# Kernel optimization log

Hardware: AMD Instinct MI355X
Metric: run time of the kernel (lower is better)

## Reference

```python
import jax, jax.numpy as jnp
import numpy as np

B, C, D = 8192, 4, 256
E, H, O = 8, 256, 128
AQ, HQ = 18, 512
THRESH = 0.3
MAX_OUT_REC = 2


def setup_inputs() -> dict:
    key = jax.random.key(0)
    ks = jax.random.split(key, 16)
    s = lambda *sh: 1.0 / np.sqrt(sh[-2] if len(sh) > 1 else sh[-1])
    inp = {
        'data': jax.random.normal(ks[0], (B, C, D), jnp.float32),
        # stacked expert MLPs: D -> H -> O
        'We1': jax.random.normal(ks[1], (E, D, H), jnp.float32) / np.sqrt(D),
        'be1': jnp.zeros((E, H), jnp.float32),
        'We2': jax.random.normal(ks[2], (E, H, O), jnp.float32) / np.sqrt(H),
        'be2': jnp.zeros((E, O), jnp.float32),
        # gating: D -> E (softmax)
        'Wg': jax.random.normal(ks[3], (D, E), jnp.float32) / np.sqrt(D),
        'bg': jnp.zeros((E,), jnp.float32),
        # outer recursive gating: C*O -> 2 (softmax)
        'Wog': jax.random.normal(ks[4], (C * O, 2), jnp.float32) / np.sqrt(C * O),
        'bog': jnp.zeros((2,), jnp.float32),
        # recursive mapping: O -> D
        'Wr': jax.random.normal(ks[5], (O, D), jnp.float32) / np.sqrt(O),
        'br': jnp.zeros((D,), jnp.float32),
        # Q network: C*O -> HQ -> A
        'Wq1': jax.random.normal(ks[6], (C * O, HQ), jnp.float32) / np.sqrt(C * O),
        'bq1': jnp.zeros((HQ,), jnp.float32),
        'Wq2': jax.random.normal(ks[7], (HQ, AQ), jnp.float32) / np.sqrt(HQ),
        'bq2': jnp.zeros((AQ,), jnp.float32),
    }
    return inp


def _moe_forward(x3, We1, be1, We2, be2, Wg, bg):
    # x3: (B, C, D) -> tokens (N, D), N = B*C
    b = x3.shape[0]
    x = x3.reshape(b * C, D)
    # dense all-experts forward
    h = jax.nn.relu(jnp.einsum('nd,edh->enh', x, We1) + be1[:, None, :])  # (E,N,H)
    eo = jnp.einsum('enh,eho->eno', h, We2) + be2[:, None, :]              # (E,N,O)
    g = jax.nn.softmax(x @ Wg + bg, axis=-1)                               # (N,E)
    out = jnp.einsum('ne,eno->no', g, eo)                                  # (N,O)
    return out.reshape(b, C * O)


def reference(data, We1, be1, We2, be2, Wg, bg, Wog, bog, Wr, br, Wq1, bq1, Wq2, bq2):
    result = _moe_forward(data, We1, be1, We2, be2, Wg, bg)               # (B, C*O)
    co = jax.nn.softmax(result @ Wog + bog, axis=-1)                      # (B, 2)
    gate2 = (co[:, 0] > THRESH).astype(result.dtype)[:, None]             # (B, 1)
    # while-loop with per-sample mask; unrolled MAX_OUT_REC iterations is
    # exact: once a sample's mask is 0 its result (hence mask) is unchanged.
    for _ in range(MAX_OUT_REC):
        r_ = result.reshape(data.shape[0] * C, O) @ Wr + br               # recursive_mapping
        r3 = r_.reshape(data.shape[0], C, D)
        out = _moe_forward(r3, We1, be1, We2, be2, Wg, bg)
        result = result + out * co[:, 0:1] * gate2
        co = jax.nn.softmax(result @ Wog + bog, axis=-1)
        gate2 = (co[:, 0] > 0.5).astype(result.dtype)[:, None]
    values = jax.nn.relu(result @ Wq1 + bq1) @ Wq2 + bq2                  # (B, A)
    return values
```

## Files before the change

kernel.cpp:

```cpp
#include <hip/hip_runtime.h>
#include <math.h>


typedef _Float16 f16;
typedef f16   f16x8  __attribute__((ext_vector_type(8)));
typedef f16   f16x4  __attribute__((ext_vector_type(4)));
typedef float f32x16 __attribute__((ext_vector_type(16)));
typedef float v4f    __attribute__((ext_vector_type(4)));

#define MFMA(a, b, c) __builtin_amdgcn_mfma_f32_32x32x16_f16(a, b, c, 0, 0, 0)
#define LO_SCALE 4096.0f
#define LO_INV   (1.0f / 4096.0f)

#define XS 264
#define RS 136
#define QS 520

__device__ __forceinline__ v4f nt_load4(const float* p) {
    return __builtin_nontemporal_load((const v4f*)p);
}

__global__ __launch_bounds__(256) void prep_kernel(
    const float* __restrict__ We1, const float* __restrict__ We2,
    const float* __restrict__ Wr,  const float* __restrict__ Wg,
    const float* __restrict__ Wq1, const float* __restrict__ Wq2,
    f16* __restrict__ W1H, f16* __restrict__ W1L,
    f16* __restrict__ W2H, f16* __restrict__ W2L,
    f16* __restrict__ WrH, f16* __restrict__ WrL,
    f16* __restrict__ WgH, f16* __restrict__ WgL,
    f16* __restrict__ Wq1H, f16* __restrict__ Wq1L,
    f16* __restrict__ Wq2H, f16* __restrict__ Wq2L)
{
    int t = blockIdx.x * 4 + (threadIdx.x >> 6);
    int lane = threadIdx.x & 63;
    const float* src; f16 *dh, *dl;
    int stride, ncols, kbase, nbase, tile;
    if (t < 1024) {
        int e = t >> 7, kt = (t >> 3) & 15, nt = t & 7;
        src = We1 + e * 65536; stride = 256; ncols = 256;
        kbase = kt * 16; nbase = nt * 32; tile = t; dh = W1H; dl = W1L;
    } else if (t < 1536) {
        int i = t - 1024; int e = i >> 6, kt = (i >> 2) & 15, nt = i & 3;
        src = We2 + e * 32768; stride = 128; ncols = 128;
        kbase = kt * 16; nbase = nt * 32; tile = i; dh = W2H; dl = W2L;
    } else if (t < 1600) {
        int i = t - 1536; int kt = i >> 3, nt = i & 7;
        src = Wr; stride = 256; ncols = 256;
        kbase = kt * 16; nbase = nt * 32; tile = i; dh = WrH; dl = WrL;
    } else if (t < 1616) {
        int i = t - 1600;
        src = Wg; stride = 8; ncols = 8;
        kbase = i * 16; nbase = 0; tile = i; dh = WgH; dl = WgL;
    } else if (t < 2128) {
        int i = t - 1616; int kt = i >> 4, nt = i & 15;
        src = Wq1; stride = 512; ncols = 512;
        kbase = kt * 16; nbase = nt * 32; tile = i; dh = Wq1H; dl = Wq1L;
    } else {
        int i = t - 2128;
        src = Wq2; stride = 18; ncols = 18;
        kbase = i * 16; nbase = 0; tile = i; dh = Wq2H; dl = Wq2L;
    }
    int n = lane & 31, kg = lane >> 5;
    int col = nbase + n;
    f16x8 hv, lv;
    #pragma unroll
    for (int j = 0; j < 8; ++j) {
        int k = kbase + kg * 8 + j;
        float w = (col < ncols) ? src[(size_t)k * stride + col] : 0.f;
        f16 h = (f16)w;
        hv[j] = h;
        lv[j] = (f16)((w - (float)h) * LO_SCALE);
    }
    *(f16x8*)(dh + (size_t)tile * 512 + lane * 8) = hv;
    *(f16x8*)(dl + (size_t)tile * 512 + lane * 8) = lv;
}

template<bool REC>
__global__ __launch_bounds__(256, 2) void moe_mfma(
    const float* xsrc, const float* __restrict__ sbuf,
    const f16* __restrict__ W1H, const f16* __restrict__ W1L,
    const f16* __restrict__ W2H, const f16* __restrict__ W2L,
    const f16* __restrict__ WrH, const f16* __restrict__ WrL,
    const f16* __restrict__ WgH, const f16* __restrict__ WgL,
    const float* __restrict__ be1, const float* __restrict__ be2,
    const float* __restrict__ bg,  const float* __restrict__ br,
    float* result)
{
    extern __shared__ char smem[];
    f16* xh = (f16*)smem;
    f16* xl = xh + 32 * XS;
    f16* hh = xl + 32 * XS;
    f16* hl = hh + 32 * XS;

    const int tid = threadIdx.x;
    const int lane = tid & 63;
    const int wv = tid >> 6;
    const int l31 = lane & 31;
    const int kg = lane >> 5;
    const int n0 = blockIdx.x * 32;

    if (!REC) {
        #pragma unroll
        for (int i = 0; i < 8; ++i) {
            int idx = i * 256 + tid;
            int m = idx >> 6, k4 = (idx & 63) * 4;
            v4f v = nt_load4(&xsrc[(size_t)(n0 + m) * 256 + k4]);
            f16x4 hv, lv;
            #pragma unroll
            for (int j = 0; j < 4; ++j) {
                hv[j] = (f16)v[j];
                lv[j] = (f16)((v[j] - (float)hv[j]) * LO_SCALE);
            }
            *(f16x4*)&xh[m * XS + k4] = hv;
            *(f16x4*)&xl[m * XS + k4] = lv;
        }
    } else {
        #pragma unroll
        for (int i = 0; i < 4; ++i) {
            int idx = i * 256 + tid;
            int m = idx >> 5, k4 = (idx & 31) * 4;
            v4f v = nt_load4(&xsrc[(size_t)(n0 + m) * 128 + k4]);
            f16x4 hv, lv;
            #pragma unroll
            for (int j = 0; j < 4; ++j) {
                hv[j] = (f16)v[j];
                lv[j] = (f16)((v[j] - (float)hv[j]) * LO_SCALE);
            }
            *(f16x4*)&hh[m * RS + k4] = hv;
            *(f16x4*)&hl[m * RS + k4] = lv;
        }
        __syncthreads();
        f32x16 am0 = {}, a0a = {}, a0b = {}, am1 = {}, a1a = {}, a1b = {};
        const f16* wrh = WrH + (size_t)(2 * wv) * 512 + lane * 8;
        const f16* wrl = WrL + (size_t)(2 * wv) * 512 + lane * 8;
        #pragma unroll
        for (int kt = 0; kt < 8; ++kt) {
            f16x8 b0h = *(const f16x8*)(wrh + (size_t)kt * 4096);
            f16x8 b0l = *(const f16x8*)(wrl + (size_t)kt * 4096);
            f16x8 b1h = *(const f16x8*)(wrh + (size_t)kt * 4096 + 512);
            f16x8 b1l = *(const f16x8*)(wrl + (size_t)kt * 4096 + 512);
            f16x8 ah = *(const f16x8*)&hh[l31 * RS + kt * 16 + kg * 8];
            f16x8 al = *(const f16x8*)&hl[l31 * RS + kt * 16 + kg * 8];
            am0 = MFMA(ah, b0h, am0); a0a = MFMA(al, b0h, a0a); a0b = MFMA(ah, b0l, a0b);
            am1 = MFMA(ah, b1h, am1); a1a = MFMA(al, b1h, a1a); a1b = MFMA(ah, b1l, a1b);
        }
        #pragma unroll
        for (int t = 0; t < 2; ++t) {
            int col = (2 * wv + t) * 32 + l31;
            float brv = br[col];
            #pragma unroll
            for (int r = 0; r < 16; ++r) {
                int row = (r & 3) + 8 * (r >> 2) + 4 * kg;
                float v = (t ? am1[r] + (a1a[r] + a1b[r]) * LO_INV
                             : am0[r] + (a0a[r] + a0b[r]) * LO_INV) + brv;
                f16 hv = (f16)v;
                xh[row * XS + col] = hv;
                xl[row * XS + col] = (f16)((v - (float)hv) * LO_SCALE);
            }
        }
    }
    __syncthreads();

    float gr[16];
    {
        f32x16 gm = {}, ga = {}, gb = {};
        #pragma unroll
        for (int kt = 0; kt < 16; ++kt) {
            f16x8 ah = *(const f16x8*)&xh[l31 * XS + kt * 16 + kg * 8];
            f16x8 al = *(const f16x8*)&xl[l31 * XS + kt * 16 + kg * 8];
            f16x8 bh = *(const f16x8*)(WgH + (size_t)kt * 512 + lane * 8);
            f16x8 bl = *(const f16x8*)(WgL + (size_t)kt * 512 + lane * 8);
            gm = MFMA(ah, bh, gm); ga = MFMA(al, bh, ga); gb = MFMA(ah, bl, gb);
        }
        float bge = (l31 < 8) ? bg[l31] : 0.f;
        #pragma unroll
        for (int r = 0; r < 16; ++r) {
            float lg = gm[r] + (ga[r] + gb[r]) * LO_INV + bge;
            float mx = lg;
            #pragma unroll
            for (int d = 1; d < 8; d <<= 1) mx = fmaxf(mx, __shfl_xor(mx, d, 64));
            float ex = __expf(lg - mx);
            float s = ex;
            #pragma unroll
            for (int d = 1; d < 8; d <<= 1) s += __shfl_xor(s, d, 64);
            gr[r] = ex / s;
        }
    }

    f32x16 out = {};
    #pragma unroll 1
    for (int e = 0; e < 8; ++e) {
        f32x16 am0 = {}, a0a = {}, a0b = {}, am1 = {}, a1a = {}, a1b = {};
        const f16* w1h = W1H + (size_t)e * 65536 + (2 * wv) * 512 + lane * 8;
        const f16* w1l = W1L + (size_t)e * 65536 + (2 * wv) * 512 + lane * 8;
        #pragma unroll
        for (int kt = 0; kt < 16; ++kt) {
            f16x8 b0h = *(const f16x8*)(w1h + (size_t)kt * 4096);
            f16x8 b0l = *(const f16x8*)(w1l + (size_t)kt * 4096);
            f16x8 b1h = *(const f16x8*)(w1h + (size_t)kt * 4096 + 512);
            f16x8 b1l = *(const f16x8*)(w1l + (size_t)kt * 4096 + 512);
            f16x8 ah = *(const f16x8*)&xh[l31 * XS + kt * 16 + kg * 8];
            f16x8 al = *(const f16x8*)&xl[l31 * XS + kt * 16 + kg * 8];
            am0 = MFMA(ah, b0h, am0); a0a = MFMA(al, b0h, a0a); a0b = MFMA(ah, b0l, a0b);
            am1 = MFMA(ah, b1h, am1); a1a = MFMA(al, b1h, a1a); a1b = MFMA(ah, b1l, a1b);
        }
        __syncthreads();
        #pragma unroll
        for (int t = 0; t < 2; ++t) {
            int col = (2 * wv + t) * 32 + l31;
            float b1v = be1[e * 256 + col];
            #pragma unroll
            for (int r = 0; r < 16; ++r) {
                int row = (r & 3) + 8 * (r >> 2) + 4 * kg;
                float v = (t ? am1[r] + (a1a[r] + a1b[r]) * LO_INV
                             : am0[r] + (a0a[r] + a0b[r]) * LO_INV) + b1v;
                v = fmaxf(v, 0.f);
                f16 hv = (f16)v;
                hh[row * XS + col] = hv;
                hl[row * XS + col] = (f16)((v - (float)hv) * LO_SCALE);
            }
        }
        __syncthreads();
        f32x16 am2 = {}, a2a = {}, a2b = {};
        const f16* w2h = W2H + (size_t)e * 32768 + wv * 512 + lane * 8;
        const f16* w2l = W2L + (size_t)e * 32768 + wv * 512 + lane * 8;
        #pragma unroll
        for (int kt = 0; kt < 16; ++kt) {
            f16x8 bh = *(const f16x8*)(w2h + (size_t)kt * 2048);
            f16x8 bl = *(const f16x8*)(w2l + (size_t)kt * 2048);
            f16x8 ah = *(const f16x8*)&hh[l31 * XS + kt * 16 + kg * 8];
            f16x8 al = *(const f16x8*)&hl[l31 * XS + kt * 16 + kg * 8];
            am2 = MFMA(ah, bh, am2); a2a = MFMA(al, bh, a2a); a2b = MFMA(ah, bl, a2b);
        }
        float be2v = be2[e * 128 + wv * 32 + l31];
        #pragma unroll
        for (int r = 0; r < 16; ++r) {
            float eo = am2[r] + (a2a[r] + a2b[r]) * LO_INV + be2v;
            float gv = __shfl(gr[r], (lane & 32) + e, 64);
            out[r] += gv * eo;
        }
    }

    int col = wv * 32 + l31;
    #pragma unroll
    for (int r = 0; r < 16; ++r) {
        int row = (r & 3) + 8 * (r >> 2) + 4 * kg;
        size_t off = (size_t)(n0 + row) * 128 + col;
        float v = out[r];
        if (REC) {
            float sv = sbuf[(n0 + row) >> 2];
            float old = __builtin_nontemporal_load(&result[off]);
            v = old + v * sv;
        }
        __builtin_nontemporal_store(v, &result[off]);
    }
}

__global__ __launch_bounds__(256) void co_kernel(
    const float* __restrict__ result, const float* __restrict__ Wog,
    const float* __restrict__ bog, float* __restrict__ sbuf, float thresh)
{
    int lane = threadIdx.x & 63;
    int w = threadIdx.x >> 6;
    int b = blockIdx.x * 4 + w;
    const float* r = result + (size_t)b * 512;
    float l0 = 0.f, l1 = 0.f;
    #pragma unroll
    for (int j = 0; j < 8; ++j) {
        int d = j * 64 + lane;
        float rv = __builtin_nontemporal_load(&r[d]);
        float2 wv = *(const float2*)&Wog[d * 2];
        l0 = fmaf(rv, wv.x, l0);
        l1 = fmaf(rv, wv.y, l1);
    }
    #pragma unroll
    for (int off = 32; off > 0; off >>= 1) {
        l0 += __shfl_down(l0, off);
        l1 += __shfl_down(l1, off);
    }
    if (lane == 0) {
        l0 += bog[0]; l1 += bog[1];
        float co0 = 1.f / (1.f + __expf(l1 - l0));
        sbuf[b] = (co0 > thresh) ? co0 : 0.f;
    }
}

__global__ __launch_bounds__(512, 2) void q_mfma(
    const float* __restrict__ result,
    const f16* __restrict__ Wq1H, const f16* __restrict__ Wq1L,
    const f16* __restrict__ Wq2H, const f16* __restrict__ Wq2L,
    const float* __restrict__ bq1, const float* __restrict__ bq2,
    float* __restrict__ out)
{
    extern __shared__ char smem[];
    f16* rh = (f16*)smem;
    f16* rl = rh + 32 * QS;
    f16* hh = rl + 32 * QS;
    f16* hl = hh + 32 * QS;
    float* part = (float*)(hl + 32 * QS);
    const int tid = threadIdx.x;
    const int lane = tid & 63;
    const int wv = tid >> 6;
    const int l31 = lane & 31;
    const int kg = lane >> 5;
    const int n0 = blockIdx.x * 32;

    #pragma unroll
    for (int i = 0; i < 8; ++i) {
        int idx = i * 512 + tid;
        int m = idx >> 7, k4 = (idx & 127) * 4;
        v4f v = nt_load4(&result[(size_t)(n0 + m) * 512 + k4]);
        f16x4 hv, lv;
        #pragma unroll
        for (int j = 0; j < 4; ++j) {
            hv[j] = (f16)v[j];
            lv[j] = (f16)((v[j] - (float)hv[j]) * LO_SCALE);
        }
        *(f16x4*)&rh[m * QS + k4] = hv;
        *(f16x4*)&rl[m * QS + k4] = lv;
    }
    __syncthreads();

    f32x16 am0 = {}, ac0 = {}, am1 = {}, ac1 = {};
    const int nt0 = wv * 2;
    #pragma unroll
    for (int kt = 0; kt < 32; ++kt) {
        f16x8 ah = *(const f16x8*)&rh[l31 * QS + kt * 16 + kg * 8];
        f16x8 al = *(const f16x8*)&rl[l31 * QS + kt * 16 + kg * 8];
        f16x8 b0h = *(const f16x8*)(Wq1H + (size_t)(kt * 16 + nt0) * 512 + lane * 8);
        f16x8 b0l = *(const f16x8*)(Wq1L + (size_t)(kt * 16 + nt0) * 512 + lane * 8);
        f16x8 b1h = *(const f16x8*)(Wq1H + (size_t)(kt * 16 + nt0 + 1) * 512 + lane * 8);
        f16x8 b1l = *(const f16x8*)(Wq1L + (size_t)(kt * 16 + nt0 + 1) * 512 + lane * 8);
        am0 = MFMA(ah, b0h, am0); ac0 = MFMA(al, b0h, ac0); ac0 = MFMA(ah, b0l, ac0);
        am1 = MFMA(ah, b1h, am1); ac1 = MFMA(al, b1h, ac1); ac1 = MFMA(ah, b1l, ac1);
    }
    #pragma unroll
    for (int t = 0; t < 2; ++t) {
        int col = (nt0 + t) * 32 + l31;
        float b1v = bq1[col];
        #pragma unroll
        for (int r = 0; r < 16; ++r) {
            int row = (r & 3) + 8 * (r >> 2) + 4 * kg;
            float v = (t ? am1[r] + ac1[r] * LO_INV : am0[r] + ac0[r] * LO_INV) + b1v;
            v = fmaxf(v, 0.f);
            f16 hv = (f16)v;
            hh[row * QS + col] = hv;
            hl[row * QS + col] = (f16)((v - (float)hv) * LO_SCALE);
        }
    }
    __syncthreads();

    if (wv < 4) {
        f32x16 am = {}, ac = {};
        #pragma unroll
        for (int k2 = 0; k2 < 8; ++k2) {
            int kt = wv * 8 + k2;
            f16x8 ah = *(const f16x8*)&hh[l31 * QS + kt * 16 + kg * 8];
            f16x8 al = *(const f16x8*)&hl[l31 * QS + kt * 16 + kg * 8];
            f16x8 bh = *(const f16x8*)(Wq2H + (size_t)kt * 512 + lane * 8);
            f16x8 bl = *(const f16x8*)(Wq2L + (size_t)kt * 512 + lane * 8);
            am = MFMA(ah, bh, am); ac = MFMA(al, bh, ac); ac = MFMA(ah, bl, ac);
        }
        #pragma unroll
        for (int r = 0; r < 16; ++r) {
            int row = (r & 3) + 8 * (r >> 2) + 4 * kg;
            part[wv * 1024 + row * 32 + l31] = am[r] + ac[r] * LO_INV;
        }
    }
    __syncthreads();
    for (int idx = tid; idx < 1024; idx += 512) {
        int row = idx >> 5, c = idx & 31;
        if (c < 18) {
            float s = part[idx] + part[1024 + idx] + part[2048 + idx] + part[3072 + idx]
                      + bq2[c];
            out[(size_t)(n0 + row) * 18 + c] = s;
        }
    }
}

extern "C" void kernel_launch(void* const* d_in, const int* in_sizes, int n_in,
                              void* d_out, int out_size, void* d_ws, size_t ws_size,
                              hipStream_t stream)
{
    (void)in_sizes; (void)n_in; (void)out_size; (void)ws_size;
    const float* data = (const float*)d_in[0];
    const float* We1  = (const float*)d_in[1];
    const float* be1  = (const float*)d_in[2];
    const float* We2  = (const float*)d_in[3];
    const float* be2  = (const float*)d_in[4];
    const float* Wg   = (const float*)d_in[5];
    const float* bg   = (const float*)d_in[6];
    const float* Wog  = (const float*)d_in[7];
    const float* bog  = (const float*)d_in[8];
    const float* Wr   = (const float*)d_in[9];
    const float* br   = (const float*)d_in[10];
    const float* Wq1  = (const float*)d_in[11];
    const float* bq1  = (const float*)d_in[12];
    const float* Wq2  = (const float*)d_in[13];
    const float* bq2  = (const float*)d_in[14];
    float* outp = (float*)d_out;

    float* result = (float*)d_ws;
    float* sbuf   = result + (size_t)32768 * 128;
    f16* fb = (f16*)((char*)d_ws + 16809984);
    f16* W1H  = fb;
    f16* W1L  = fb + 524288;
    f16* W2H  = fb + 1048576;
    f16* W2L  = fb + 1310720;
    f16* WrH  = fb + 1572864;
    f16* WrL  = fb + 1605632;
    f16* WgH  = fb + 1638400;
    f16* WgL  = fb + 1646592;
    f16* Wq1H = fb + 1654784;
    f16* Wq1L = fb + 1916928;
    f16* Wq2H = fb + 2179072;
    f16* Wq2L = fb + 2195456;

    const int MOE_LDS = 4 * 32 * XS * 2;
    const int Q_LDS   = 4 * 32 * QS * 2 + 4 * 1024 * 4;

    prep_kernel<<<540, 256, 0, stream>>>(We1, We2, Wr, Wg, Wq1, Wq2,
        W1H, W1L, W2H, W2L, WrH, WrL, WgH, WgL, Wq1H, Wq1L, Wq2H, Wq2L);

    moe_mfma<false><<<1024, 256, MOE_LDS, stream>>>(
        data, nullptr, W1H, W1L, W2H, W2L, WrH, WrL, WgH, WgL,
        be1, be2, bg, br, result);
    co_kernel<<<2048, 256, 0, stream>>>(result, Wog, bog, sbuf, 0.3f);
    moe_mfma<true><<<1024, 256, MOE_LDS, stream>>>(
        result, sbuf, W1H, W1L, W2H, W2L, WrH, WrL, WgH, WgL,
        be1, be2, bg, br, result);
    co_kernel<<<2048, 256, 0, stream>>>(result, Wog, bog, sbuf, 0.5f);
    moe_mfma<true><<<1024, 256, MOE_LDS, stream>>>(
        result, sbuf, W1H, W1L, W2H, W2L, WrH, WrL, WgH, WgL,
        be1, be2, bg, br, result);
    q_mfma<<<256, 512, Q_LDS, stream>>>(result, Wq1H, Wq1L, Wq2H, Wq2L,
        bq1, bq2, outp);
}
```

Before: 739.5 us.

## Keep expert hidden activations in registers via transposed GEMM and cross-wave reduction

The first expert GEMM is computed transposed (weights as A operand, tokens as B), so each wave's hidden-unit slice can be repacked in registers with lane shuffles into the A operand of the second GEMM. This removes the LDS round trip for the hidden activations and the two barriers per expert. Each wave now produces partial sums over its own hidden-unit K slice for all output columns, and these are reduced across the four waves through LDS at the end. The cost is more accumulator registers (four 32x32 output tiles per wave) and a final cross-wave reduction; LDS use drops, which may allow higher occupancy.

```diff
diff --git a/kernel.cpp b/kernel.cpp
--- a/kernel.cpp
+++ b/kernel.cpp
@@ -7,6 +7,7 @@
 typedef f16   f16x4  __attribute__((ext_vector_type(4)));
 typedef float f32x16 __attribute__((ext_vector_type(16)));
 typedef float v4f    __attribute__((ext_vector_type(4)));
+typedef unsigned int v4u __attribute__((ext_vector_type(4)));
 
 #define MFMA(a, b, c) __builtin_amdgcn_mfma_f32_32x32x16_f16(a, b, c, 0, 0, 0)
 #define LO_SCALE 4096.0f
@@ -18,6 +19,14 @@
 
 __device__ __forceinline__ v4f nt_load4(const float* p) {
     return __builtin_nontemporal_load((const v4f*)p);
+}
+__device__ __forceinline__ f16x8 ldg8(const f16* p) {
+    return *(const f16x8*)p;
+}
+__device__ __forceinline__ unsigned f16pack(f16 h, f16 l) {
+    union { f16 f; unsigned short s; } a, b;
+    a.f = h; b.f = l;
+    return (unsigned)a.s | ((unsigned)b.s << 16);
 }
 
 __global__ __launch_bounds__(256) void prep_kernel(
@@ -89,8 +98,7 @@
     extern __shared__ char smem[];
     f16* xh = (f16*)smem;
     f16* xl = xh + 32 * XS;
-    f16* hh = xl + 32 * XS;
-    f16* hl = hh + 32 * XS;
+    float* red = (float*)(xl + 32 * XS);
 
     const int tid = threadIdx.x;
     const int lane = tid & 63;
@@ -115,6 +123,8 @@
             *(f16x4*)&xl[m * XS + k4] = lv;
         }
     } else {
+        f16* rh = (f16*)red;
+        f16* rl = rh + 32 * RS;
         #pragma unroll
         for (int i = 0; i < 4; ++i) {
             int idx = i * 256 + tid;
@@ -126,8 +136,8 @@
                 hv[j] = (f16)v[j];
                 lv[j] = (f16)((v[j] - (float)hv[j]) * LO_SCALE);
             }
-            *(f16x4*)&hh[m * RS + k4] = hv;
-            *(f16x4*)&hl[m * RS + k4] = lv;
+            *(f16x4*)&rh[m * RS + k4] = hv;
+            *(f16x4*)&rl[m * RS + k4] = lv;
         }
         __syncthreads();
         f32x16 am0 = {}, a0a = {}, a0b = {}, am1 = {}, a1a = {}, a1b = {};
@@ -135,12 +145,12 @@
         const f16* wrl = WrL + (size_t)(2 * wv) * 512 + lane * 8;
         #pragma unroll
         for (int kt = 0; kt < 8; ++kt) {
-            f16x8 b0h = *(const f16x8*)(wrh + (size_t)kt * 4096);
-            f16x8 b0l = *(const f16x8*)(wrl + (size_t)kt * 4096);
-            f16x8 b1h = *(const f16x8*)(wrh + (size_t)kt * 4096 + 512);
-            f16x8 b1l = *(const f16x8*)(wrl + (size_t)kt * 4096 + 512);
-            f16x8 ah = *(const f16x8*)&hh[l31 * RS + kt * 16 + kg * 8];
-            f16x8 al = *(const f16x8*)&hl[l31 * RS + kt * 16 + kg * 8];
+            f16x8 b0h = ldg8(wrh + (size_t)kt * 4096);
+            f16x8 b0l = ldg8(wrl + (size_t)kt * 4096);
+            f16x8 b1h = ldg8(wrh + (size_t)kt * 4096 + 512);
+            f16x8 b1l = ldg8(wrl + (size_t)kt * 4096 + 512);
+            f16x8 ah = *(const f16x8*)&rh[l31 * RS + kt * 16 + kg * 8];
+            f16x8 al = *(const f16x8*)&rl[l31 * RS + kt * 16 + kg * 8];
             am0 = MFMA(ah, b0h, am0); a0a = MFMA(al, b0h, a0a); a0b = MFMA(ah, b0l, a0b);
             am1 = MFMA(ah, b1h, am1); a1a = MFMA(al, b1h, a1a); a1b = MFMA(ah, b1l, a1b);
         }
@@ -168,8 +178,8 @@
         for (int kt = 0; kt < 16; ++kt) {
             f16x8 ah = *(const f16x8*)&xh[l31 * XS + kt * 16 + kg * 8];
             f16x8 al = *(const f16x8*)&xl[l31 * XS + kt * 16 + kg * 8];
-            f16x8 bh = *(const f16x8*)(WgH + (size_t)kt * 512 + lane * 8);
-            f16x8 bl = *(const f16x8*)(WgL + (size_t)kt * 512 + lane * 8);
+            f16x8 bh = ldg8(WgH + (size_t)kt * 512 + lane * 8);
+            f16x8 bl = ldg8(WgL + (size_t)kt * 512 + lane * 8);
             gm = MFMA(ah, bh, gm); ga = MFMA(al, bh, ga); gb = MFMA(ah, bl, gb);
         }
         float bge = (l31 < 8) ? bg[l31] : 0.f;
@@ -187,7 +197,7 @@
         }
     }
 
-    f32x16 out = {};
+    f32x16 out[4] = {};
     #pragma unroll 1
     for (int e = 0; e < 8; ++e) {
         f32x16 am0 = {}, a0a = {}, a0b = {}, am1 = {}, a1a = {}, a1b = {};
@@ -195,64 +205,136 @@
         const f16* w1l = W1L + (size_t)e * 65536 + (2 * wv) * 512 + lane * 8;
         #pragma unroll
         for (int kt = 0; kt < 16; ++kt) {
-            f16x8 b0h = *(const f16x8*)(w1h + (size_t)kt * 4096);
-            f16x8 b0l = *(const f16x8*)(w1l + (size_t)kt * 4096);
-            f16x8 b1h = *(const f16x8*)(w1h + (size_t)kt * 4096 + 512);
-            f16x8 b1l = *(const f16x8*)(w1l + (size_t)kt * 4096 + 512);
-            f16x8 ah = *(const f16x8*)&xh[l31 * XS + kt * 16 + kg * 8];
-            f16x8 al = *(const f16x8*)&xl[l31 * XS + kt * 16 + kg * 8];
-            am0 = MFMA(ah, b0h, am0); a0a = MFMA(al, b0h, a0a); a0b = MFMA(ah, b0l, a0b);
-            am1 = MFMA(ah, b1h, am1); a1a = MFMA(al, b1h, a1a); a1b = MFMA(ah, b1l, a1b);
-        }
-        __syncthreads();
-        #pragma unroll
-        for (int t = 0; t < 2; ++t) {
-            int col = (2 * wv + t) * 32 + l31;
-            float b1v = be1[e * 256 + col];
+            f16x8 a0h = ldg8(w1h + (size_t)kt * 4096);
+            f16x8 a0l = ldg8(w1l + (size_t)kt * 4096);
+            f16x8 a1h = ldg8(w1h + (size_t)kt * 4096 + 512);
+            f16x8 a1l = ldg8(w1l + (size_t)kt * 4096 + 512);
+            f16x8 bh = *(const f16x8*)&xh[l31 * XS + kt * 16 + kg * 8];
+            f16x8 bl = *(const f16x8*)&xl[l31 * XS + kt * 16 + kg * 8];
+            am0 = MFMA(a0h, bh, am0); a0a = MFMA(a0l, bh, a0a); a0b = MFMA(a0h, bl, a0b);
+            am1 = MFMA(a1h, bh, am1); a1a = MFMA(a1l, bh, a1a); a1b = MFMA(a1h, bl, a1b);
+        }
+        unsigned pk0[16], pk1[16];
+        #pragma unroll
+        for (int r = 0; r < 16; ++r) {
+            int rho = (r & 3) + 8 * (r >> 2) + 4 * kg;
+            float v0 = am0[r] + (a0a[r] + a0b[r]) * LO_INV
+                       + be1[e * 256 + 64 * wv + rho];
+            v0 = fmaxf(v0, 0.f);
+            f16 h0 = (f16)v0;
+            pk0[r] = f16pack(h0, (f16)((v0 - (float)h0) * LO_SCALE));
+            float v1 = am1[r] + (a1a[r] + a1b[r]) * LO_INV
+                       + be1[e * 256 + 64 * wv + 32 + rho];
+            v1 = fmaxf(v1, 0.f);
+            f16 h1 = (f16)v1;
+            pk1[r] = f16pack(h1, (f16)((v1 - (float)h1) * LO_SCALE));
+        }
+        f16x8 A2h[4], A2l[4];
+        #pragma unroll
+        for (int t2l = 0; t2l < 4; ++t2l) {
+            const unsigned* pk = (t2l >> 1) ? pk1 : pk0;
+            int ktl = t2l & 1;
+            unsigned jl[4], jh[4];
+            #pragma unroll
+            for (int c = 0; c < 4; ++c) {
+                unsigned pa = pk[c + 8 * ktl];
+                unsigned pb = pk[c + 8 * ktl + 4];
+                unsigned sa = (unsigned)__shfl_xor((int)pa, 32, 64);
+                unsigned sb = (unsigned)__shfl_xor((int)pb, 32, 64);
+                jl[c] = kg ? sb : pa;
+                jh[c] = kg ? pb : sa;
+            }
+            v4u wh, wl;
+            wh[0] = (jl[0] & 0xffffu) | (jl[1] << 16);
+            wh[1] = (jl[2] & 0xffffu) | (jl[3] << 16);
+            wh[2] = (jh[0] & 0xffffu) | (jh[1] << 16);
+            wh[3] = (jh[2] & 0xffffu) | (jh[3] << 16);
+            wl[0] = (jl[0] >> 16) | (jl[1] & 0xffff0000u);
+            wl[1] = (jl[2] >> 16) | (jl[3] & 0xffff0000u);
+            wl[2] = (jh[0] >> 16) | (jh[1] & 0xffff0000u);
+            wl[3] = (jh[2] >> 16) | (jh[3] & 0xffff0000u);
+            A2h[t2l] = __builtin_bit_cast(f16x8, wh);
+            A2l[t2l] = __builtin_bit_cast(f16x8, wl);
+        }
+        float ge[16];
+        #pragma unroll
+        for (int r = 0; r < 16; ++r)
+            ge[r] = __shfl(gr[r], (lane & 32) + e, 64);
+        #pragma unroll
+        for (int nt = 0; nt < 4; ++nt) {
+            f32x16 cm = {}, ca = {}, cb = {};
+            const f16* w2h = W2H + (size_t)e * 32768 + (size_t)(4 * wv * 4 + nt) * 512
+                             + lane * 8;
+            const f16* w2l = W2L + (size_t)e * 32768 + (size_t)(4 * wv * 4 + nt) * 512
+                             + lane * 8;
+            #pragma unroll
+            for (int t2l = 0; t2l < 4; ++t2l) {
+                f16x8 bh = ldg8(w2h + (size_t)t2l * 2048);
+                f16x8 bl = ldg8(w2l + (size_t)t2l * 2048);
+                cm = MFMA(A2h[t2l], bh, cm);
+                ca = MFMA(A2l[t2l], bh, ca);
+                cb = MFMA(A2h[t2l], bl, cb);
+            }
+            float be2v = (wv == 0) ? be2[e * 128 + nt * 32 + l31] : 0.f;
+            #pragma unroll
+            for (int r = 0; r < 16; ++r) {
+                float tmp = cm[r] + (ca[r] + cb[r]) * LO_INV + be2v;
+                out[nt][r] += ge[r] * tmp;
+            }
+        }
+    }
+
+    if (wv >= 2) {
+        float* dst = red + (wv - 2) * 4096;
+        #pragma unroll
+        for (int nt = 0; nt < 4; ++nt)
+            #pragma unroll
+            for (int r = 0; r < 16; ++r)
+                dst[nt * 1024 + r * 64 + lane] = out[nt][r];
+    }
+    __syncthreads();
+    if (wv < 2) {
+        const float* src = red + wv * 4096;
+        #pragma unroll
+        for (int nt = 0; nt < 4; ++nt)
+            #pragma unroll
+            for (int r = 0; r < 16; ++r)
+                out[nt][r] += src[nt * 1024 + r * 64 + lane];
+    }
+    __syncthreads();
+    if (wv == 0) {
+        #pragma unroll
+        for (int nt = 2; nt < 4; ++nt)
+            #pragma unroll
+            for (int r = 0; r < 16; ++r)
+                red[(nt - 2) * 1024 + r * 64 + lane] = out[nt][r];
+    } else if (wv == 1) {
+        #pragma unroll
+        for (int nt = 0; nt < 2; ++nt)
+            #pragma unroll
+            for (int r = 0; r < 16; ++r)
+                red[2048 + nt * 1024 + r * 64 + lane] = out[nt][r];
+    }
+    __syncthreads();
+    if (wv < 2) {
+        #pragma unroll
+        for (int q = 0; q < 2; ++q) {
+            int nt = wv * 2 + q;
+            const float* src = (wv == 0) ? (red + 2048 + nt * 1024)
+                                         : (red + (nt - 2) * 1024);
             #pragma unroll
             for (int r = 0; r < 16; ++r) {
                 int row = (r & 3) + 8 * (r >> 2) + 4 * kg;
-                float v = (t ? am1[r] + (a1a[r] + a1b[r]) * LO_INV
-                             : am0[r] + (a0a[r] + a0b[r]) * LO_INV) + b1v;
-                v = fmaxf(v, 0.f);
-                f16 hv = (f16)v;
-                hh[row * XS + col] = hv;
-                hl[row * XS + col] = (f16)((v - (float)hv) * LO_SCALE);
-            }
-        }
-        __syncthreads();
-        f32x16 am2 = {}, a2a = {}, a2b = {};
-        const f16* w2h = W2H + (size_t)e * 32768 + wv * 512 + lane * 8;
-        const f16* w2l = W2L + (size_t)e * 32768 + wv * 512 + lane * 8;
-        #pragma unroll
-        for (int kt = 0; kt < 16; ++kt) {
-            f16x8 bh = *(const f16x8*)(w2h + (size_t)kt * 2048);
-            f16x8 bl = *(const f16x8*)(w2l + (size_t)kt * 2048);
-            f16x8 ah = *(const f16x8*)&hh[l31 * XS + kt * 16 + kg * 8];
-            f16x8 al = *(const f16x8*)&hl[l31 * XS + kt * 16 + kg * 8];
-            am2 = MFMA(ah, bh, am2); a2a = MFMA(al, bh, a2a); a2b = MFMA(ah, bl, a2b);
-        }
-        float be2v = be2[e * 128 + wv * 32 + l31];
-        #pragma unroll
-        for (int r = 0; r < 16; ++r) {
-            float eo = am2[r] + (a2a[r] + a2b[r]) * LO_INV + be2v;
-            float gv = __shfl(gr[r], (lane & 32) + e, 64);
-            out[r] += gv * eo;
-        }
-    }
-
-    int col = wv * 32 + l31;
-    #pragma unroll
-    for (int r = 0; r < 16; ++r) {
-        int row = (r & 3) + 8 * (r >> 2) + 4 * kg;
-        size_t off = (size_t)(n0 + row) * 128 + col;
-        float v = out[r];
-        if (REC) {
-            float sv = sbuf[(n0 + row) >> 2];
-            float old = __builtin_nontemporal_load(&result[off]);
-            v = old + v * sv;
-        }
-        __builtin_nontemporal_store(v, &result[off]);
+                size_t off = (size_t)(n0 + row) * 128 + nt * 32 + l31;
+                float v = out[nt][r] + src[r * 64 + lane];
+                if (REC) {
+                    float sv = sbuf[(n0 + row) >> 2];
+                    float old = __builtin_nontemporal_load(&result[off]);
+                    v = old + v * sv;
+                }
+                __builtin_nontemporal_store(v, &result[off]);
+            }
+        }
     }
 }
 
@@ -327,10 +409,10 @@
     for (int kt = 0; kt < 32; ++kt) {
         f16x8 ah = *(const f16x8*)&rh[l31 * QS + kt * 16 + kg * 8];
         f16x8 al = *(const f16x8*)&rl[l31 * QS + kt * 16 + kg * 8];
-        f16x8 b0h = *(const f16x8*)(Wq1H + (size_t)(kt * 16 + nt0) * 512 + lane * 8);
-        f16x8 b0l = *(const f16x8*)(Wq1L + (size_t)(kt * 16 + nt0) * 512 + lane * 8);
-        f16x8 b1h = *(const f16x8*)(Wq1H + (size_t)(kt * 16 + nt0 + 1) * 512 + lane * 8);
-        f16x8 b1l = *(const f16x8*)(Wq1L + (size_t)(kt * 16 + nt0 + 1) * 512 + lane * 8);
+        f16x8 b0h = ldg8(Wq1H + (size_t)(kt * 16 + nt0) * 512 + lane * 8);
+        f16x8 b0l = ldg8(Wq1L + (size_t)(kt * 16 + nt0) * 512 + lane * 8);
+        f16x8 b1h = ldg8(Wq1H + (size_t)(kt * 16 + nt0 + 1) * 512 + lane * 8);
+        f16x8 b1l = ldg8(Wq1L + (size_t)(kt * 16 + nt0 + 1) * 512 + lane * 8);
         am0 = MFMA(ah, b0h, am0); ac0 = MFMA(al, b0h, ac0); ac0 = MFMA(ah, b0l, ac0);
         am1 = MFMA(ah, b1h, am1); ac1 = MFMA(al, b1h, ac1); ac1 = MFMA(ah, b1l, ac1);
     }
@@ -357,8 +439,8 @@
             int kt = wv * 8 + k2;
             f16x8 ah = *(const f16x8*)&hh[l31 * QS + kt * 16 + kg * 8];
             f16x8 al = *(const f16x8*)&hl[l31 * QS + kt * 16 + kg * 8];
-            f16x8 bh = *(const f16x8*)(Wq2H + (size_t)kt * 512 + lane * 8);
-            f16x8 bl = *(const f16x8*)(Wq2L + (size_t)kt * 512 + lane * 8);
+            f16x8 bh = ldg8(Wq2H + (size_t)kt * 512 + lane * 8);
+            f16x8 bl = ldg8(Wq2L + (size_t)kt * 512 + lane * 8);
             am = MFMA(ah, bh, am); ac = MFMA(al, bh, ac); ac = MFMA(ah, bl, ac);
         }
         #pragma unroll
@@ -416,7 +498,7 @@
     f16* Wq2H = fb + 2179072;
     f16* Wq2L = fb + 2195456;
 
-    const int MOE_LDS = 4 * 32 * XS * 2;
+    const int MOE_LDS = 2 * 32 * XS * 2 + 32768;
     const int Q_LDS   = 4 * 32 * QS * 2 + 4 * 1024 * 4;
 
     prep_kernel<<<540, 256, 0, stream>>>(We1, We2, Wr, Wg, Wq1, Wq2,
```

Result: slower. 2.190 ms (+196.1%).

## Use 8 waves per MoE block with split-K second GEMM and LDS reduction

Applied to the files above, without the earlier changes.

The MoE kernel now runs 512 threads (8 waves) per 32-token block instead of 4 waves. Each wave computes one 32-column tile of the first-layer and recursive-mapping GEMMs, while the second-layer GEMM is split over K across two wave halves and combined through an LDS reduction. The correction MFMAs now share one accumulator instead of two, which cuts register pressure so occupancy can rise (launch bounds 512,4). The cost is extra barriers and an LDS reduction pass, and the gate GEMM is still computed redundantly by every wave.

```diff
diff --git a/kernel.cpp b/kernel.cpp
--- a/kernel.cpp
+++ b/kernel.cpp
@@ -18,6 +18,9 @@
 
 __device__ __forceinline__ v4f nt_load4(const float* p) {
     return __builtin_nontemporal_load((const v4f*)p);
+}
+__device__ __forceinline__ f16x8 ldg8(const f16* p) {
+    return *(const f16x8*)p;
 }
 
 __global__ __launch_bounds__(256) void prep_kernel(
@@ -76,7 +79,7 @@
 }
 
 template<bool REC>
-__global__ __launch_bounds__(256, 2) void moe_mfma(
+__global__ __launch_bounds__(512, 4) void moe_mfma(
     const float* xsrc, const float* __restrict__ sbuf,
     const f16* __restrict__ W1H, const f16* __restrict__ W1L,
     const f16* __restrict__ W2H, const f16* __restrict__ W2L,
@@ -98,11 +101,12 @@
     const int l31 = lane & 31;
     const int kg = lane >> 5;
     const int n0 = blockIdx.x * 32;
+    const int nt2 = wv & 3, kh = wv >> 2;
 
     if (!REC) {
         #pragma unroll
-        for (int i = 0; i < 8; ++i) {
-            int idx = i * 256 + tid;
+        for (int i = 0; i < 4; ++i) {
+            int idx = i * 512 + tid;
             int m = idx >> 6, k4 = (idx & 63) * 4;
             v4f v = nt_load4(&xsrc[(size_t)(n0 + m) * 256 + k4]);
             f16x4 hv, lv;
@@ -115,9 +119,11 @@
             *(f16x4*)&xl[m * XS + k4] = lv;
         }
     } else {
-        #pragma unroll
-        for (int i = 0; i < 4; ++i) {
-            int idx = i * 256 + tid;
+        f16* rh = hh;
+        f16* rl = hl;
+        #pragma unroll
+        for (int i = 0; i < 2; ++i) {
+            int idx = i * 512 + tid;
             int m = idx >> 5, k4 = (idx & 31) * 4;
             v4f v = nt_load4(&xsrc[(size_t)(n0 + m) * 128 + k4]);
             f16x4 hv, lv;
@@ -126,33 +132,28 @@
                 hv[j] = (f16)v[j];
                 lv[j] = (f16)((v[j] - (float)hv[j]) * LO_SCALE);
             }
-            *(f16x4*)&hh[m * RS + k4] = hv;
-            *(f16x4*)&hl[m * RS + k4] = lv;
+            *(f16x4*)&rh[m * RS + k4] = hv;
+            *(f16x4*)&rl[m * RS + k4] = lv;
         }
         __syncthreads();
-        f32x16 am0 = {}, a0a = {}, a0b = {}, am1 = {}, a1a = {}, a1b = {};
-        const f16* wrh = WrH + (size_t)(2 * wv) * 512 + lane * 8;
-        const f16* wrl = WrL + (size_t)(2 * wv) * 512 + lane * 8;
+        f32x16 am = {}, ac = {};
+        const f16* wrh = WrH + (size_t)wv * 512 + lane * 8;
+        const f16* wrl = WrL + (size_t)wv * 512 + lane * 8;
         #pragma unroll
         for (int kt = 0; kt < 8; ++kt) {
-            f16x8 b0h = *(const f16x8*)(wrh + (size_t)kt * 4096);
-            f16x8 b0l = *(const f16x8*)(wrl + (size_t)kt * 4096);
-            f16x8 b1h = *(const f16x8*)(wrh + (size_t)kt * 4096 + 512);
-            f16x8 b1l = *(const f16x8*)(wrl + (size_t)kt * 4096 + 512);
-            f16x8 ah = *(const f16x8*)&hh[l31 * RS + kt * 16 + kg * 8];
-            f16x8 al = *(const f16x8*)&hl[l31 * RS + kt * 16 + kg * 8];
-            am0 = MFMA(ah, b0h, am0); a0a = MFMA(al, b0h, a0a); a0b = MFMA(ah, b0l, a0b);
-            am1 = MFMA(ah, b1h, am1); a1a = MFMA(al, b1h, a1a); a1b = MFMA(ah, b1l, a1b);
-        }
-        #pragma unroll
-        for (int t = 0; t < 2; ++t) {
-            int col = (2 * wv + t) * 32 + l31;
+            f16x8 bh = ldg8(wrh + (size_t)kt * 4096);
+            f16x8 bl = ldg8(wrl + (size_t)kt * 4096);
+            f16x8 ah = *(const f16x8*)&rh[l31 * RS + kt * 16 + kg * 8];
+            f16x8 al = *(const f16x8*)&rl[l31 * RS + kt * 16 + kg * 8];
+            am = MFMA(ah, bh, am); ac = MFMA(al, bh, ac); ac = MFMA(ah, bl, ac);
+        }
+        {
+            int col = wv * 32 + l31;
             float brv = br[col];
             #pragma unroll
             for (int r = 0; r < 16; ++r) {
                 int row = (r & 3) + 8 * (r >> 2) + 4 * kg;
-                float v = (t ? am1[r] + (a1a[r] + a1b[r]) * LO_INV
-                             : am0[r] + (a0a[r] + a0b[r]) * LO_INV) + brv;
+                float v = am[r] + ac[r] * LO_INV + brv;
                 f16 hv = (f16)v;
                 xh[row * XS + col] = hv;
                 xl[row * XS + col] = (f16)((v - (float)hv) * LO_SCALE);
@@ -163,19 +164,19 @@
 
     float gr[16];
     {
-        f32x16 gm = {}, ga = {}, gb = {};
+        f32x16 gm = {}, gc = {};
         #pragma unroll
         for (int kt = 0; kt < 16; ++kt) {
+            f16x8 bh = ldg8(WgH + (size_t)kt * 512 + lane * 8);
+            f16x8 bl = ldg8(WgL + (size_t)kt * 512 + lane * 8);
             f16x8 ah = *(const f16x8*)&xh[l31 * XS + kt * 16 + kg * 8];
             f16x8 al = *(const f16x8*)&xl[l31 * XS + kt * 16 + kg * 8];
-            f16x8 bh = *(const f16x8*)(WgH + (size_t)kt * 512 + lane * 8);
-            f16x8 bl = *(const f16x8*)(WgL + (size_t)kt * 512 + lane * 8);
-            gm = MFMA(ah, bh, gm); ga = MFMA(al, bh, ga); gb = MFMA(ah, bl, gb);
+            gm = MFMA(ah, bh, gm); gc = MFMA(al, bh, gc); gc = MFMA(ah, bl, gc);
         }
         float bge = (l31 < 8) ? bg[l31] : 0.f;
         #pragma unroll
         for (int r = 0; r < 16; ++r) {
-            float lg = gm[r] + (ga[r] + gb[r]) * LO_INV + bge;
+            float lg = gm[r] + gc[r] * LO_INV + bge;
             float mx = lg;
             #pragma unroll
             for (int d = 1; d < 8; d <<= 1) mx = fmaxf(mx, __shfl_xor(mx, d, 64));
@@ -190,30 +191,25 @@
     f32x16 out = {};
     #pragma unroll 1
     for (int e = 0; e < 8; ++e) {
-        f32x16 am0 = {}, a0a = {}, a0b = {}, am1 = {}, a1a = {}, a1b = {};
-        const f16* w1h = W1H + (size_t)e * 65536 + (2 * wv) * 512 + lane * 8;
-        const f16* w1l = W1L + (size_t)e * 65536 + (2 * wv) * 512 + lane * 8;
+        f32x16 am = {}, ac = {};
+        const f16* w1h = W1H + (size_t)e * 65536 + (size_t)wv * 512 + lane * 8;
+        const f16* w1l = W1L + (size_t)e * 65536 + (size_t)wv * 512 + lane * 8;
         #pragma unroll
         for (int kt = 0; kt < 16; ++kt) {
-            f16x8 b0h = *(const f16x8*)(w1h + (size_t)kt * 4096);
-            f16x8 b0l = *(const f16x8*)(w1l + (size_t)kt * 4096);
-            f16x8 b1h = *(const f16x8*)(w1h + (size_t)kt * 4096 + 512);
-            f16x8 b1l = *(const f16x8*)(w1l + (size_t)kt * 4096 + 512);
+            f16x8 bh = ldg8(w1h + (size_t)kt * 4096);
+            f16x8 bl = ldg8(w1l + (size_t)kt * 4096);
             f16x8 ah = *(const f16x8*)&xh[l31 * XS + kt * 16 + kg * 8];
             f16x8 al = *(const f16x8*)&xl[l31 * XS + kt * 16 + kg * 8];
-            am0 = MFMA(ah, b0h, am0); a0a = MFMA(al, b0h, a0a); a0b = MFMA(ah, b0l, a0b);
-            am1 = MFMA(ah, b1h, am1); a1a = MFMA(al, b1h, a1a); a1b = MFMA(ah, b1l, a1b);
+            am = MFMA(ah, bh, am); ac = MFMA(al, bh, ac); ac = MFMA(ah, bl, ac);
         }
         __syncthreads();
-        #pragma unroll
-        for (int t = 0; t < 2; ++t) {
-            int col = (2 * wv + t) * 32 + l31;
+        {
+            int col = wv * 32 + l31;
             float b1v = be1[e * 256 + col];
             #pragma unroll
             for (int r = 0; r < 16; ++r) {
                 int row = (r & 3) + 8 * (r >> 2) + 4 * kg;
-                float v = (t ? am1[r] + (a1a[r] + a1b[r]) * LO_INV
-                             : am0[r] + (a0a[r] + a0b[r]) * LO_INV) + b1v;
+                float v = am[r] + ac[r] * LO_INV + b1v;
                 v = fmaxf(v, 0.f);
                 f16 hv = (f16)v;
                 hh[row * XS + col] = hv;
@@ -221,38 +217,49 @@
             }
         }
         __syncthreads();
-        f32x16 am2 = {}, a2a = {}, a2b = {};
-        const f16* w2h = W2H + (size_t)e * 32768 + wv * 512 + lane * 8;
-        const f16* w2l = W2L + (size_t)e * 32768 + wv * 512 + lane * 8;
-        #pragma unroll
-        for (int kt = 0; kt < 16; ++kt) {
-            f16x8 bh = *(const f16x8*)(w2h + (size_t)kt * 2048);
-            f16x8 bl = *(const f16x8*)(w2l + (size_t)kt * 2048);
+        f32x16 am2 = {}, ac2 = {};
+        const f16* w2h = W2H + (size_t)e * 32768 + (size_t)nt2 * 512 + lane * 8;
+        const f16* w2l = W2L + (size_t)e * 32768 + (size_t)nt2 * 512 + lane * 8;
+        #pragma unroll
+        for (int k2 = 0; k2 < 8; ++k2) {
+            int kt = kh * 8 + k2;
+            f16x8 bh = ldg8(w2h + (size_t)kt * 2048);
+            f16x8 bl = ldg8(w2l + (size_t)kt * 2048);
             f16x8 ah = *(const f16x8*)&hh[l31 * XS + kt * 16 + kg * 8];
             f16x8 al = *(const f16x8*)&hl[l31 * XS + kt * 16 + kg * 8];
-            am2 = MFMA(ah, bh, am2); a2a = MFMA(al, bh, a2a); a2b = MFMA(ah, bl, a2b);
-        }
-        float be2v = be2[e * 128 + wv * 32 + l31];
+            am2 = MFMA(ah, bh, am2); ac2 = MFMA(al, bh, ac2); ac2 = MFMA(ah, bl, ac2);
+        }
+        float be2v = (kh == 0) ? be2[e * 128 + nt2 * 32 + l31] : 0.f;
         #pragma unroll
         for (int r = 0; r < 16; ++r) {
-            float eo = am2[r] + (a2a[r] + a2b[r]) * LO_INV + be2v;
+            float eo = am2[r] + ac2[r] * LO_INV + be2v;
             float gv = __shfl(gr[r], (lane & 32) + e, 64);
             out[r] += gv * eo;
         }
     }
 
-    int col = wv * 32 + l31;
-    #pragma unroll
-    for (int r = 0; r < 16; ++r) {
-        int row = (r & 3) + 8 * (r >> 2) + 4 * kg;
-        size_t off = (size_t)(n0 + row) * 128 + col;
-        float v = out[r];
-        if (REC) {
-            float sv = sbuf[(n0 + row) >> 2];
-            float old = __builtin_nontemporal_load(&result[off]);
-            v = old + v * sv;
-        }
-        __builtin_nontemporal_store(v, &result[off]);
+    float* red = (float*)hh;
+    __syncthreads();
+    if (kh == 1) {
+        #pragma unroll
+        for (int r = 0; r < 16; ++r)
+            red[nt2 * 1024 + r * 64 + lane] = out[r];
+    }
+    __syncthreads();
+    if (kh == 0) {
+        int col = nt2 * 32 + l31;
+        #pragma unroll
+        for (int r = 0; r < 16; ++r) {
+            int row = (r & 3) + 8 * (r >> 2) + 4 * kg;
+            size_t off = (size_t)(n0 + row) * 128 + col;
+            float v = out[r] + red[nt2 * 1024 + r * 64 + lane];
+            if (REC) {
+                float sv = sbuf[(n0 + row) >> 2];
+                float old = __builtin_nontemporal_load(&result[off]);
+                v = old + v * sv;
+            }
+            __builtin_nontemporal_store(v, &result[off]);
+        }
     }
 }
 
@@ -327,10 +334,10 @@
     for (int kt = 0; kt < 32; ++kt) {
         f16x8 ah = *(const f16x8*)&rh[l31 * QS + kt * 16 + kg * 8];
         f16x8 al = *(const f16x8*)&rl[l31 * QS + kt * 16 + kg * 8];
-        f16x8 b0h = *(const f16x8*)(Wq1H + (size_t)(kt * 16 + nt0) * 512 + lane * 8);
-        f16x8 b0l = *(const f16x8*)(Wq1L + (size_t)(kt * 16 + nt0) * 512 + lane * 8);
-        f16x8 b1h = *(const f16x8*)(Wq1H + (size_t)(kt * 16 + nt0 + 1) * 512 + lane * 8);
-        f16x8 b1l = *(const f16x8*)(Wq1L + (size_t)(kt * 16 + nt0 + 1) * 512 + lane * 8);
+        f16x8 b0h = ldg8(Wq1H + (size_t)(kt * 16 + nt0) * 512 + lane * 8);
+        f16x8 b0l = ldg8(Wq1L + (size_t)(kt * 16 + nt0) * 512 + lane * 8);
+        f16x8 b1h = ldg8(Wq1H + (size_t)(kt * 16 + nt0 + 1) * 512 + lane * 8);
+        f16x8 b1l = ldg8(Wq1L + (size_t)(kt * 16 + nt0 + 1) * 512 + lane * 8);
         am0 = MFMA(ah, b0h, am0); ac0 = MFMA(al, b0h, ac0); ac0 = MFMA(ah, b0l, ac0);
         am1 = MFMA(ah, b1h, am1); ac1 = MFMA(al, b1h, ac1); ac1 = MFMA(ah, b1l, ac1);
     }
@@ -357,8 +364,8 @@
             int kt = wv * 8 + k2;
             f16x8 ah = *(const f16x8*)&hh[l31 * QS + kt * 16 + kg * 8];
             f16x8 al = *(const f16x8*)&hl[l31 * QS + kt * 16 + kg * 8];
-            f16x8 bh = *(const f16x8*)(Wq2H + (size_t)kt * 512 + lane * 8);
-            f16x8 bl = *(const f16x8*)(Wq2L + (size_t)kt * 512 + lane * 8);
+            f16x8 bh = ldg8(Wq2H + (size_t)kt * 512 + lane * 8);
+            f16x8 bl = ldg8(Wq2L + (size_t)kt * 512 + lane * 8);
             am = MFMA(ah, bh, am); ac = MFMA(al, bh, ac); ac = MFMA(ah, bl, ac);
         }
         #pragma unroll
@@ -422,15 +429,15 @@
     prep_kernel<<<540, 256, 0, stream>>>(We1, We2, Wr, Wg, Wq1, Wq2,
         W1H, W1L, W2H, W2L, WrH, WrL, WgH, WgL, Wq1H, Wq1L, Wq2H, Wq2L);
 
-    moe_mfma<false><<<1024, 256, MOE_LDS, stream>>>(
+    moe_mfma<false><<<1024, 512, MOE_LDS, stream>>>(
         data, nullptr, W1H, W1L, W2H, W2L, WrH, WrL, WgH, WgL,
         be1, be2, bg, br, result);
     co_kernel<<<2048, 256, 0, stream>>>(result, Wog, bog, sbuf, 0.3f);
-    moe_mfma<true><<<1024, 256, MOE_LDS, stream>>>(
+    moe_mfma<true><<<1024, 512, MOE_LDS, stream>>>(
         result, sbuf, W1H, W1L, W2H, W2L, WrH, WrL, WgH, WgL,
         be1, be2, bg, br, result);
     co_kernel<<<2048, 256, 0, stream>>>(result, Wog, bog, sbuf, 0.5f);
-    moe_mfma<true><<<1024, 256, MOE_LDS, stream>>>(
+    moe_mfma<true><<<1024, 512, MOE_LDS, stream>>>(
         result, sbuf, W1H, W1L, W2H, W2L, WrH, WrL, WgH, WgL,
         be1, be2, bg, br, result);
     q_mfma<<<256, 512, Q_LDS, stream>>>(result, Wq1H, Wq1L, Wq2H, Wq2L,
```

After: 720.5 us. 2.6% less time.
